# Kernel tuning notes

Measured on AMD Instinct MI355X. Metric: run time of the kernel, lower is better.

## Reference

```python
import jax, jax.numpy as jnp
import numpy as np

B, T, E, H = 16, 4096, 384, 64

def setup_inputs() -> dict:
    key = jax.random.key(0)
    k1, k2, k3, k4 = jax.random.split(key, 4)
    x = jax.random.normal(k1, (B, T, E), dtype=jnp.float32)
    # nn.Linear default init ~ U(-1/sqrt(fan_in), 1/sqrt(fan_in)); scale normals similarly
    s = 1.0 / np.sqrt(E)
    Wk = jax.random.uniform(k2, (E, H), dtype=jnp.float32, minval=-s, maxval=s)
    Wq = jax.random.uniform(k3, (E, H), dtype=jnp.float32, minval=-s, maxval=s)
    Wv = jax.random.uniform(k4, (E, H), dtype=jnp.float32, minval=-s, maxval=s)
    return {"x": x, "Wk": Wk, "Wq": Wq, "Wv": Wv}

def reference(x, Wk, Wq, Wv):
    b, t, c = x.shape
    k = x @ Wk          # [b,t,h]
    q = x @ Wq          # [b,t,h]
    v = x @ Wv          # [b,t,h]
    # scale by C**-0.5 where C is the embedding dim (as in source)
    scale = c ** (-0.5)
    weights = jnp.einsum('bqh,bkh->bqk', q, k) * scale  # [b,t,t]
    causal = jnp.tril(jnp.ones((t, t), dtype=bool))
    weights = jnp.where(causal, weights, -jnp.inf)
    weights = jax.nn.softmax(weights, axis=-1)
    # dropout is identity in eval mode
    out = jnp.einsum('bqk,bkh->bqh', weights, v)          # [b,t,h]
    return out
```

## Files before the change

### kernel.cpp

```cpp
#include <hip/hip_runtime.h>
#include <hip/hip_bf16.h>
#include <math.h>


typedef __attribute__((ext_vector_type(4))) float f32x4;
typedef __attribute__((ext_vector_type(8))) __bf16 bf16x8;

#define DEVI static __device__ __forceinline__

DEVI unsigned short f2bf(float f) {
  union { float f; unsigned int u; } x; x.f = f;
  unsigned int r = x.u + 0x7fffu + ((x.u >> 16) & 1u);
  return (unsigned short)(r >> 16);
}

DEVI unsigned int cvtpk_bf16(float lo, float hi) {
  unsigned int r;
  asm("v_cvt_pk_bf16_f32 %0, %1, %2" : "=v"(r) : "v"(lo), "v"(hi));
  return r;
}

DEVI f32x4 mfma16(bf16x8 a, bf16x8 b, f32x4 c) {
  return __builtin_amdgcn_mfma_f32_16x16x32_bf16(a, b, c, 0, 0, 0);
}

DEVI bf16x8 lds_frag(const unsigned short* buf, int row, int gran) {
  return *(const bf16x8*)(buf + row * 64 + ((gran ^ (row & 7)) << 3));
}

DEVI void gl_lds16(const unsigned short* g, unsigned short* l) {
  __builtin_amdgcn_global_load_lds(
      (const __attribute__((address_space(1))) unsigned int*)g,
      (__attribute__((address_space(3))) unsigned int*)l, 16, 0, 0);
}

__global__ __launch_bounds__(256) void k_pack(const float* __restrict__ Wk,
                                              const float* __restrict__ Wq,
                                              const float* __restrict__ Wv,
                                              unsigned short* __restrict__ WT) {
  int idx = blockIdx.x * 256 + threadIdx.x;
  if (idx >= 192 * 384) return;
  int n = idx / 384, k = idx - n * 384;
  const float* W = (n < 64) ? Wk : ((n < 128) ? Wq : Wv);
  WT[idx] = f2bf(W[k * 64 + (n & 63)]);
}

__global__ __launch_bounds__(256, 4) void k_proj(const float* __restrict__ x,
                                                 const unsigned short* __restrict__ WT,
                                                 unsigned short* __restrict__ Y,
                                                 unsigned short* __restrict__ VT) {
  __shared__ __align__(16) unsigned short As[64 * 64];
  __shared__ __align__(16) unsigned short Bs[192 * 64];
  const int tid = threadIdx.x;
  const int lane = tid & 63, wid = tid >> 6;
  const int q = lane & 15, g = lane >> 4;
  const int wm = wid >> 1, wn = wid & 1;
  const int m0 = blockIdx.x * 64;

  f32x4 acc[2][6];
#pragma unroll
  for (int mt = 0; mt < 2; ++mt)
#pragma unroll
    for (int nt = 0; nt < 6; ++nt) acc[mt][nt] = f32x4{0.f, 0.f, 0.f, 0.f};

  const int ar = tid >> 2, ap = tid & 3;

  for (int ks = 0; ks < 6; ++ks) {
    const float4* xp = (const float4*)(x + (size_t)(m0 + ar) * 384 + ks * 64 + ap * 16);
#pragma unroll
    for (int cc = 0; cc < 2; ++cc) {
      float4 f0 = xp[cc * 2], f1 = xp[cc * 2 + 1];
      union { unsigned short h[8]; uint4 v; } u;
      u.h[0] = f2bf(f0.x); u.h[1] = f2bf(f0.y); u.h[2] = f2bf(f0.z); u.h[3] = f2bf(f0.w);
      u.h[4] = f2bf(f1.x); u.h[5] = f2bf(f1.y); u.h[6] = f2bf(f1.z); u.h[7] = f2bf(f1.w);
      int gran = ap * 2 + cc;
      *(uint4*)(As + ar * 64 + ((gran ^ (ar & 7)) << 3)) = u.v;
    }
#pragma unroll
    for (int i = 0; i < 6; ++i) {
      int c = tid + 256 * i;
      int row = c >> 3, gr = c & 7;
      uint4 w = *(const uint4*)(WT + (size_t)row * 384 + ks * 64 + gr * 8);
      *(uint4*)(Bs + row * 64 + ((gr ^ (row & 7)) << 3)) = w;
    }
    __syncthreads();
#pragma unroll
    for (int kk = 0; kk < 2; ++kk) {
      bf16x8 af[2], bfv[6];
#pragma unroll
      for (int mt = 0; mt < 2; ++mt) af[mt] = lds_frag(As, wm * 32 + mt * 16 + q, kk * 4 + g);
#pragma unroll
      for (int nt = 0; nt < 6; ++nt) bfv[nt] = lds_frag(Bs, wn * 96 + nt * 16 + q, kk * 4 + g);
#pragma unroll
      for (int mt = 0; mt < 2; ++mt)
#pragma unroll
        for (int nt = 0; nt < 6; ++nt) acc[mt][nt] = mfma16(af[mt], bfv[nt], acc[mt][nt]);
    }
    __syncthreads();
  }
#pragma unroll
  for (int mt = 0; mt < 2; ++mt) {
    const int mrow = m0 + wm * 32 + mt * 16 + g * 4;
#pragma unroll
    for (int nt = 0; nt < 6; ++nt) {
      const int ncol = wn * 96 + nt * 16 + q;
      if (wn == 1 && nt >= 2) {
        const int d = (nt - 2) * 16 + q;
        const int bb = mrow >> 12, t = mrow & 4095;
        uint2 pv;
        pv.x = cvtpk_bf16(acc[mt][nt][0], acc[mt][nt][1]);
        pv.y = cvtpk_bf16(acc[mt][nt][2], acc[mt][nt][3]);
        *(uint2*)(VT + (size_t)(bb * 64 + d) * 4096 + t) = pv;
      } else {
        size_t base = (size_t)mrow * 128 + ncol;
#pragma unroll
        for (int j = 0; j < 4; ++j) Y[base + (size_t)j * 128] = f2bf(acc[mt][nt][j]);
      }
    }
  }
}

__global__ __launch_bounds__(512, 4) void k_attn(const unsigned short* __restrict__ Y,
                                                 const unsigned short* __restrict__ VT,
                                                 float* __restrict__ out) {
  __shared__ __align__(16) unsigned short Ks[4][64 * 64];
  __shared__ __align__(16) unsigned short Vs[4][64 * 64];
  __shared__ __align__(16) unsigned short Ps[8][16 * 64];

  const int flat = blockIdx.x;
  const int xcd = flat & 7, idx = flat >> 3;
  const int b = xcd * 2 + (idx >> 5);
  const int pr = idx & 31;

  const int tid = threadIdx.x;
  const int lane = tid & 63, wid = tid >> 6;
  const int p = wid >> 2;
  const int w4 = wid & 3;
  const int q = lane & 15, g = lane >> 4;
  const float zsc = 0.073622223f;

  const unsigned short* Yb = Y + (size_t)b * 4096 * 128;
  const unsigned short* Vb = VT + (size_t)b * 64 * 4096;

#define STAGE(S, KV0)                                                           \
  {                                                                             \
    int r = tid >> 3, grs = (tid & 7) ^ (r & 7);                                \
    gl_lds16(Yb + (size_t)((KV0) + r) * 128 + grs * 8, Ks[S] + tid * 8);        \
    gl_lds16(Vb + (size_t)r * 4096 + (KV0) + grs * 8, Vs[S] + tid * 8);         \
  }

  int q0 = (63 - pr) * 64, nkv = 64 - pr;
  STAGE(0, 0)
  STAGE(1, 64)
  __syncthreads();

  for (int phase = 0; phase < 2; ++phase) {
    const int qrow = q0 + w4 * 16 + q;
    const unsigned short* qp = Yb + (size_t)qrow * 128 + 64;
    bf16x8 qf0 = *(const bf16x8*)(qp + g * 8);
    bf16x8 qf1 = *(const bf16x8*)(qp + 32 + g * 8);
#pragma unroll
    for (int e = 0; e < 8; ++e) {
      qf0[e] = (__bf16)((float)qf0[e] * zsc);
      qf1[e] = (__bf16)((float)qf1[e] * zsc);
    }

    f32x4 accO[4];
#pragma unroll
    for (int dt = 0; dt < 4; ++dt) accO[dt] = f32x4{0.f, 0.f, 0.f, 0.f};
    float lsum = 0.f;

    const int nIt = (nkv + 1) >> 1;
    for (int it = 0; it < nIt; ++it) {
      const int kt = 2 * it + p;
      const int t2 = 2 * it + 2, t3 = 2 * it + 3;
      if (t2 < nkv) STAGE(t2 & 3, t2 * 64)
      if (t3 < nkv) STAGE(t3 & 3, t3 * 64)

      if (kt < nkv) {
        const int kv0 = kt * 64;
        const unsigned short* Kc = Ks[kt & 3];
        const unsigned short* Vc = Vs[kt & 3];

        bf16x8 ka0[4], ka1[4];
#pragma unroll
        for (int t = 0; t < 4; ++t) {
          ka0[t] = lds_frag(Kc, t * 16 + q, g);
          ka1[t] = lds_frag(Kc, t * 16 + q, 4 + g);
        }
        f32x4 accS[4];
        __builtin_amdgcn_s_setprio(1);
#pragma unroll
        for (int t = 0; t < 4; ++t) {
          f32x4 z = f32x4{0.f, 0.f, 0.f, 0.f};
          z = mfma16(ka0[t], qf0, z);
          z = mfma16(ka1[t], qf1, z);
          accS[t] = z;
        }
        __builtin_amdgcn_s_setprio(0);

        if (kt == nkv - 1) {
#pragma unroll
          for (int t = 0; t < 4; ++t)
#pragma unroll
            for (int j = 0; j < 4; ++j)
              if (kv0 + t * 16 + g * 4 + j > qrow) accS[t][j] = -INFINITY;
        }
        float ps0 = 0.f, ps1 = 0.f;
#pragma unroll
        for (int t = 0; t < 4; ++t) {
          float p0 = __builtin_amdgcn_exp2f(accS[t][0]);
          float p1 = __builtin_amdgcn_exp2f(accS[t][1]);
          float p2 = __builtin_amdgcn_exp2f(accS[t][2]);
          float p3 = __builtin_amdgcn_exp2f(accS[t][3]);
          ps0 += p0 + p1;
          ps1 += p2 + p3;
          uint2 pv;
          pv.x = cvtpk_bf16(p0, p1);
          pv.y = cvtpk_bf16(p2, p3);
          *(uint2*)(Ps[wid] + q * 64 + ((t * 16 + g * 4) ^ ((q & 7) << 3))) = pv;
        }
        lsum += ps0 + ps1;

        bf16x8 av0[4], av1[4];
#pragma unroll
        for (int dt = 0; dt < 4; ++dt) {
          av0[dt] = lds_frag(Vc, dt * 16 + q, g);
          av1[dt] = lds_frag(Vc, dt * 16 + q, 4 + g);
        }
        bf16x8 bp0 = lds_frag(Ps[wid], q, g);
        bf16x8 bp1 = lds_frag(Ps[wid], q, 4 + g);
        __builtin_amdgcn_s_setprio(1);
#pragma unroll
        for (int dt = 0; dt < 4; ++dt) {
          accO[dt] = mfma16(av0[dt], bp0, accO[dt]);
          accO[dt] = mfma16(av1[dt], bp1, accO[dt]);
        }
        __builtin_amdgcn_s_setprio(0);
      }

      __syncthreads();
    }

    lsum += __shfl_xor(lsum, 16);
    lsum += __shfl_xor(lsum, 32);

    const int nkvB = pr + 1;
    if (phase == 0) {
      STAGE(0, 0)
      if (nkvB > 1) STAGE(1, 64)
    }

    float* scrO = (float*)Ks[2];
    float* scrL = (float*)Vs[2];
    const int si = w4 * 64 + lane;
    if (p == 1) {
      float* so = scrO + si * 16;
#pragma unroll
      for (int dt = 0; dt < 4; ++dt) *(float4*)(so + dt * 4) = *(float4*)&accO[dt];
      scrL[si] = lsum;
    }
    __syncthreads();
    if (p == 0) {
      const float* so = scrO + si * 16;
      float rl = 1.0f / (lsum + scrL[si]);
      float* op = out + (size_t)(b * 4096 + qrow) * 64;
#pragma unroll
      for (int dt = 0; dt < 4; ++dt) {
        float4 ob = *(const float4*)(so + dt * 4);
        f32x4 vO;
        vO[0] = (accO[dt][0] + ob.x) * rl;
        vO[1] = (accO[dt][1] + ob.y) * rl;
        vO[2] = (accO[dt][2] + ob.z) * rl;
        vO[3] = (accO[dt][3] + ob.w) * rl;
        *(float4*)(op + dt * 16 + g * 4) = *(float4*)&vO;
      }
    }
    __syncthreads();

    q0 = pr * 64;
    nkv = nkvB;
  }
#undef STAGE
}

extern "C" void kernel_launch(void* const* d_in, const int* in_sizes, int n_in,
                              void* d_out, int out_size, void* d_ws, size_t ws_size,
                              hipStream_t stream) {
  const float* x  = (const float*)d_in[0];
  const float* Wk = (const float*)d_in[1];
  const float* Wq = (const float*)d_in[2];
  const float* Wv = (const float*)d_in[3];
  float* out = (float*)d_out;

  unsigned short* WT = (unsigned short*)d_ws;
  unsigned short* Y  = WT + 73728;
  unsigned short* VT = Y + 8388608;

  hipLaunchKernelGGL(k_pack, dim3(288), dim3(256), 0, stream, Wk, Wq, Wv, WT);
  hipLaunchKernelGGL(k_proj, dim3(1024), dim3(256), 0, stream, x, WT, Y, VT);
  hipLaunchKernelGGL(k_attn, dim3(512), dim3(512), 0, stream, Y, VT, out);
}
```

Baseline: 89.49 us.

## Switch attention blocks to 128-row query tiles with per-wave two-subtile reuse

```diff
diff --git a/kernel.cpp b/kernel.cpp
--- a/kernel.cpp
+++ b/kernel.cpp
@@ -127,10 +127,13 @@
   __shared__ __align__(16) unsigned short Vs[4][64 * 64];
   __shared__ __align__(16) unsigned short Ps[8][16 * 64];
 
-  const int flat = blockIdx.x;
-  const int xcd = flat & 7, idx = flat >> 3;
-  const int b = xcd * 2 + (idx >> 5);
-  const int pr = idx & 31;
+  const int id = blockIdx.x;
+  const int xcd = id & 7;
+  const int b = xcd * 2 + ((id >> 3) & 1);
+  const int rank = id >> 4;
+  const int i = (rank < 16) ? (31 - rank) : (rank - 16);
+  const int q0 = i * 128;
+  const int nkv = 2 * i + 2;
 
   const int tid = threadIdx.x;
   const int lane = tid & 63, wid = tid >> 6;
@@ -149,70 +152,83 @@
     gl_lds16(Vb + (size_t)r * 4096 + (KV0) + grs * 8, Vs[S] + tid * 8);         \
   }
 
-  int q0 = (63 - pr) * 64, nkv = 64 - pr;
   STAGE(0, 0)
   STAGE(1, 64)
   __syncthreads();
 
-  for (int phase = 0; phase < 2; ++phase) {
-    const int qrow = q0 + w4 * 16 + q;
-    const unsigned short* qp = Yb + (size_t)qrow * 128 + 64;
-    bf16x8 qf0 = *(const bf16x8*)(qp + g * 8);
-    bf16x8 qf1 = *(const bf16x8*)(qp + 32 + g * 8);
+  bf16x8 qf[2][2];
+#pragma unroll
+  for (int qh = 0; qh < 2; ++qh) {
+    const unsigned short* qp = Yb + (size_t)(q0 + w4 * 32 + qh * 16 + q) * 128 + 64;
+    bf16x8 r0 = *(const bf16x8*)(qp + g * 8);
+    bf16x8 r1 = *(const bf16x8*)(qp + 32 + g * 8);
 #pragma unroll
     for (int e = 0; e < 8; ++e) {
-      qf0[e] = (__bf16)((float)qf0[e] * zsc);
-      qf1[e] = (__bf16)((float)qf1[e] * zsc);
-    }
-
-    f32x4 accO[4];
-#pragma unroll
-    for (int dt = 0; dt < 4; ++dt) accO[dt] = f32x4{0.f, 0.f, 0.f, 0.f};
-    float lsum = 0.f;
-
-    const int nIt = (nkv + 1) >> 1;
-    for (int it = 0; it < nIt; ++it) {
-      const int kt = 2 * it + p;
-      const int t2 = 2 * it + 2, t3 = 2 * it + 3;
-      if (t2 < nkv) STAGE(t2 & 3, t2 * 64)
-      if (t3 < nkv) STAGE(t3 & 3, t3 * 64)
-
-      if (kt < nkv) {
-        const int kv0 = kt * 64;
-        const unsigned short* Kc = Ks[kt & 3];
-        const unsigned short* Vc = Vs[kt & 3];
-
-        bf16x8 ka0[4], ka1[4];
-#pragma unroll
-        for (int t = 0; t < 4; ++t) {
-          ka0[t] = lds_frag(Kc, t * 16 + q, g);
-          ka1[t] = lds_frag(Kc, t * 16 + q, 4 + g);
-        }
-        f32x4 accS[4];
-        __builtin_amdgcn_s_setprio(1);
+      r0[e] = (__bf16)((float)r0[e] * zsc);
+      r1[e] = (__bf16)((float)r1[e] * zsc);
+    }
+    qf[qh][0] = r0; qf[qh][1] = r1;
+  }
+
+  f32x4 accO[2][4];
+#pragma unroll
+  for (int qh = 0; qh < 2; ++qh)
+#pragma unroll
+    for (int dt = 0; dt < 4; ++dt) accO[qh][dt] = f32x4{0.f, 0.f, 0.f, 0.f};
+  float lsum[2] = {0.f, 0.f};
+
+  const int mytiles = 2 * i + 1 + (w4 >> 1);
+  const int nIt = nkv >> 1;
+
+  for (int it = 0; it < nIt; ++it) {
+    const int kt = 2 * it + p;
+    const int t2 = 2 * it + 2, t3 = 2 * it + 3;
+    if (t2 < nkv) STAGE(t2 & 3, t2 * 64)
+    if (t3 < nkv) STAGE(t3 & 3, t3 * 64)
+
+    if (kt < mytiles) {
+      const int kv0 = kt * 64;
+      const unsigned short* Kc = Ks[kt & 3];
+      const unsigned short* Vc = Vs[kt & 3];
+
+      bf16x8 ka0[4], ka1[4];
+#pragma unroll
+      for (int t = 0; t < 4; ++t) {
+        ka0[t] = lds_frag(Kc, t * 16 + q, g);
+        ka1[t] = lds_frag(Kc, t * 16 + q, 4 + g);
+      }
+      f32x4 accS[2][4];
+      __builtin_amdgcn_s_setprio(1);
+#pragma unroll
+      for (int qh = 0; qh < 2; ++qh)
 #pragma unroll
         for (int t = 0; t < 4; ++t) {
           f32x4 z = f32x4{0.f, 0.f, 0.f, 0.f};
-          z = mfma16(ka0[t], qf0, z);
-          z = mfma16(ka1[t], qf1, z);
-          accS[t] = z;
+          z = mfma16(ka0[t], qf[qh][0], z);
+          z = mfma16(ka1[t], qf[qh][1], z);
+          accS[qh][t] = z;
         }
-        __builtin_amdgcn_s_setprio(0);
-
-        if (kt == nkv - 1) {
+      __builtin_amdgcn_s_setprio(0);
+
+      const bool dmw = (kv0 + 63 >= q0 + w4 * 32);
+      bf16x8 bp[2][2];
+#pragma unroll
+      for (int qh = 0; qh < 2; ++qh) {
+        const int qrow = q0 + w4 * 32 + qh * 16 + q;
+        if (dmw) {
 #pragma unroll
           for (int t = 0; t < 4; ++t)
 #pragma unroll
             for (int j = 0; j < 4; ++j)
-              if (kv0 + t * 16 + g * 4 + j > qrow) accS[t][j] = -INFINITY;
+              if (kv0 + t * 16 + g * 4 + j > qrow) accS[qh][t][j] = -INFINITY;
         }
         float ps0 = 0.f, ps1 = 0.f;
 #pragma unroll
         for (int t = 0; t < 4; ++t) {
-          float p0 = __builtin_amdgcn_exp2f(accS[t][0]);
-          float p1 = __builtin_amdgcn_exp2f(accS[t][1]);
-          float p2 = __builtin_amdgcn_exp2f(accS[t][2]);
-          float p3 = __builtin_amdgcn_exp2f(accS[t][3]);
+          float p0 = __builtin_amdgcn_exp2f(accS[qh][t][0]);
+          float p1 = __builtin_amdgcn_exp2f(accS[qh][t][1]);
+          float p2 = __builtin_amdgcn_exp2f(accS[qh][t][2]);
+          float p3 = __builtin_amdgcn_exp2f(accS[qh][t][3]);
           ps0 += p0 + p1;
           ps1 += p2 + p3;
           uint2 pv;
@@ -220,66 +236,65 @@
           pv.y = cvtpk_bf16(p2, p3);
           *(uint2*)(Ps[wid] + q * 64 + ((t * 16 + g * 4) ^ ((q & 7) << 3))) = pv;
         }
-        lsum += ps0 + ps1;
-
-        bf16x8 av0[4], av1[4];
-#pragma unroll
-        for (int dt = 0; dt < 4; ++dt) {
-          av0[dt] = lds_frag(Vc, dt * 16 + q, g);
-          av1[dt] = lds_frag(Vc, dt * 16 + q, 4 + g);
+        lsum[qh] += ps0 + ps1;
+        bp[qh][0] = lds_frag(Ps[wid], q, g);
+        bp[qh][1] = lds_frag(Ps[wid], q, 4 + g);
+      }
+
+      __builtin_amdgcn_s_setprio(1);
+#pragma unroll
+      for (int dt = 0; dt < 4; ++dt) {
+        bf16x8 av0 = lds_frag(Vc, dt * 16 + q, g);
+        bf16x8 av1 = lds_frag(Vc, dt * 16 + q, 4 + g);
+#pragma unroll
+        for (int qh = 0; qh < 2; ++qh) {
+          accO[qh][dt] = mfma16(av0, bp[qh][0], accO[qh][dt]);
+          accO[qh][dt] = mfma16(av1, bp[qh][1], accO[qh][dt]);
         }
-        bf16x8 bp0 = lds_frag(Ps[wid], q, g);
-        bf16x8 bp1 = lds_frag(Ps[wid], q, 4 + g);
-        __builtin_amdgcn_s_setprio(1);
-#pragma unroll
-        for (int dt = 0; dt < 4; ++dt) {
-          accO[dt] = mfma16(av0[dt], bp0, accO[dt]);
-          accO[dt] = mfma16(av1[dt], bp1, accO[dt]);
-        }
-        __builtin_amdgcn_s_setprio(0);
-      }
-
-      __syncthreads();
-    }
-
-    lsum += __shfl_xor(lsum, 16);
-    lsum += __shfl_xor(lsum, 32);
-
-    const int nkvB = pr + 1;
-    if (phase == 0) {
-      STAGE(0, 0)
-      if (nkvB > 1) STAGE(1, 64)
-    }
-
-    float* scrO = (float*)Ks[2];
-    float* scrL = (float*)Vs[2];
-    const int si = w4 * 64 + lane;
-    if (p == 1) {
-      float* so = scrO + si * 16;
-#pragma unroll
-      for (int dt = 0; dt < 4; ++dt) *(float4*)(so + dt * 4) = *(float4*)&accO[dt];
-      scrL[si] = lsum;
-    }
+      }
+      __builtin_amdgcn_s_setprio(0);
+    }
+
     __syncthreads();
-    if (p == 0) {
-      const float* so = scrO + si * 16;
-      float rl = 1.0f / (lsum + scrL[si]);
+  }
+
+#pragma unroll
+  for (int qh = 0; qh < 2; ++qh) {
+    lsum[qh] += __shfl_xor(lsum[qh], 16);
+    lsum[qh] += __shfl_xor(lsum[qh], 32);
+  }
+
+  float* scrO = (float*)Ks;
+  float* scrL = (float*)Vs;
+  const int si = w4 * 64 + lane;
+  if (p == 1) {
+#pragma unroll
+    for (int qh = 0; qh < 2; ++qh) {
+      float* so = scrO + (si * 2 + qh) * 16;
+#pragma unroll
+      for (int dt = 0; dt < 4; ++dt) *(float4*)(so + dt * 4) = *(float4*)&accO[qh][dt];
+      scrL[si * 2 + qh] = lsum[qh];
+    }
+  }
+  __syncthreads();
+  if (p == 0) {
+#pragma unroll
+    for (int qh = 0; qh < 2; ++qh) {
+      const float* so = scrO + (si * 2 + qh) * 16;
+      float rl = 1.0f / (lsum[qh] + scrL[si * 2 + qh]);
+      const int qrow = q0 + w4 * 32 + qh * 16 + q;
       float* op = out + (size_t)(b * 4096 + qrow) * 64;
 #pragma unroll
       for (int dt = 0; dt < 4; ++dt) {
         float4 ob = *(const float4*)(so + dt * 4);
         f32x4 vO;
-        vO[0] = (accO[dt][0] + ob.x) * rl;
-        vO[1] = (accO[dt][1] + ob.y) * rl;
-        vO[2] = (accO[dt][2] + ob.z) * rl;
-        vO[3] = (accO[dt][3] + ob.w) * rl;
+        vO[0] = (accO[qh][dt][0] + ob.x) * rl;
+        vO[1] = (accO[qh][dt][1] + ob.y) * rl;
+        vO[2] = (accO[qh][dt][2] + ob.z) * rl;
+        vO[3] = (accO[qh][dt][3] + ob.w) * rl;
         *(float4*)(op + dt * 16 + g * 4) = *(float4*)&vO;
       }
     }
-    __syncthreads();
-
-    q0 = pr * 64;
-    nkv = nkvB;
   }
 #undef STAGE
 }
```

Result: no change. 90.83 us (+1.5%).
